# Kernel optimization log

Hardware: AMD Instinct MI355X
Metric: run time of the kernel (lower is better)

The kernel has to match this reference:

```python
import jax, jax.numpy as jnp
import numpy as np

LAG = 13
B = 32
N = 1200
NUM = 0  # self.num at call time (module starts at the init value)
H = 1.0 / 3.0


def gamma_fn(x):
    # Gamma function valid for positive and negative non-integer args
    # (reflection formula for x<0), elementwise, fp32-safe.
    xp = jnp.where(x > 0, x, jnp.float32(1.0))
    pos = jnp.exp(jax.lax.lgamma(xp))
    xn = jnp.where(x > 0, jnp.float32(0.5), x)
    neg = jnp.pi / (jnp.sin(jnp.pi * xn) * jnp.exp(jax.lax.lgamma(1.0 - xn)))
    return jnp.where(x > 0, pos, neg)


def aggregate(A, WW):
    # Fused form of: repeat_interleave -> view -> mul(WW) -> sum(dim=2) -> tanh(-x)
    # v0[l,b,i,j,e] = A[l,b,i,e]; out[l,b,j,e] = tanh(-sum_i WW[i,j,e]*A[l,b,i,e])
    return jnp.tanh(-jnp.einsum('lbie,ije->lbje', A, WW))


def setup_inputs() -> dict:
    key = jax.random.key(0)
    k = jax.random.split(key, 7)
    A = jax.random.normal(k[0], (LAG - 1, B, N, 1), jnp.float32)
    WW = jax.random.normal(k[1], (N, N, 1), jnp.float32) * 0.03
    train_init = jax.random.uniform(k[2], (B, N, LAG, 2), jnp.float32)
    alpha = jax.random.uniform(k[3], (LAG - 1, 1), jnp.float32) * 0.6 + 0.2
    fract = jax.random.uniform(k[4], (LAG - 1, 1), jnp.float32) * 0.6 + 0.2
    lambd = jax.random.normal(k[5], (LAG - 1, 1, N // 6, 1), jnp.float32) * 0.1
    l = jax.random.normal(k[6], (LAG - 1, 1, N // 6, 1), jnp.float32) * 0.1
    A_y_list = jnp.zeros((12, B, LAG - 1, N, 1), jnp.float32)
    return {"A": A, "WW": WW, "train_init": train_init, "alpha": alpha,
            "fract": fract, "lambd": lambd, "l": l, "A_y_list": A_y_list}


def reference(A, WW, train_init, alpha, fract, lambd, l, A_y_list):
    # __init__-time precomputation of A_N_OLD / A_0_NEW
    A_N_OLD = aggregate(jnp.transpose(train_init[..., :LAG - 1, 1], (2, 0, 1))[..., None], WW)
    A_0_NEW = aggregate(jnp.transpose(train_init[..., 1:LAG, 1], (2, 0, 1))[..., None], WW)

    out = aggregate(A, WW)                                   # [lag-1,B,N,1]
    A_y_list = A_y_list.at[NUM].set(jnp.transpose(out, (1, 0, 2, 3)))

    # D(): the original overwrites num=0 inside D, so only the m=0 GL term
    # survives; binom(fract,0)=Gamma(f+1)/(Gamma(1)Gamma(f+1)).
    binom0 = gamma_fn(fract + 1.0) / (gamma_fn(jnp.ones_like(fract)) * gamma_fn(fract + 1.0))
    sum_GL = A_y_list[0] * binom0[None, :, None, :]          # [B,lag-1,N,1]
    output_final_A = sum_GL / (H ** fract[None, :, None, :])

    # belta_result = sum_{k=0..3} Gamma(a+1)/(Gamma(k+1)Gamma(a-k+1))
    g_a1 = gamma_fn(alpha + 1.0)                             # [lag-1,1]
    belta_result = jnp.zeros((LAG - 1, 1), jnp.float32)
    for kk in range(4):
        kf = jnp.full((LAG - 1, 1), float(kk), jnp.float32)
        belta_result = belta_result + g_a1 / (gamma_fn(kf + 1.0) * gamma_fn(alpha - kf + 1.0))

    tmp1 = g_a1[:, None, None, :]                            # Gamma(a+1), == tmp3
    tmp2 = gamma_fn(jnp.ones((LAG - 1, 1), jnp.float32))[:, None, None, :]   # Gamma(1)=1
    tmp4 = gamma_fn(jnp.full((LAG - 1, 1), 4.0, jnp.float32))[:, None, None, :]  # Gamma(4)=6
    tmp5 = gamma_fn(alpha - 2.0)[:, None, None, :]           # Gamma(a-3+1)

    l_rep = jnp.tile(l, (1, B, 6, 1))                        # [lag-1,B,N,1]
    constant = l_rep * (tmp1 / (tmp2 * tmp1) * A_0_NEW + tmp1 / (tmp4 * tmp5) * A_N_OLD) / H
    constant = jnp.transpose(constant, (1, 0, 2, 3))         # [B,lag-1,N,1]

    lambd_rep = jnp.transpose(jnp.tile(lambd, (1, B, 6, 1)), (1, 0, 2, 3))
    return lambd_rep / belta_result[None, :, None, :] * (2.0 * output_final_A + constant)
```

## Files before the change

### kernel.cpp

```cpp
#include <hip/hip_runtime.h>
#include <math.h>

#define PI_F 3.14159265358979323846f

typedef __attribute__((ext_vector_type(8))) short bh8;
typedef __attribute__((ext_vector_type(4))) float f32x4;

#define LAG1 12
#define BB   32
#define NN   1200
#define KPAD 1216
#define NPAD 1216
#define NITER 19
#define KS0   10
#define LDSW  72


#define ROW_I4 (KPAD / 8)
#define PA_BLK 228
#define PB_BLK 150
#define PD_BLK 6
#define PC_BLK 1444
#define PE_BLK 1
#define PREP_BLOCKS (PA_BLK + PB_BLK + PD_BLK + PC_BLK + PE_BLK)

__device__ __forceinline__ unsigned short f2bf(float f) {
    unsigned int u = __float_as_uint(f);
    u = (u + 0x7fffu + ((u >> 16) & 1u)) >> 16;
    return (unsigned short)u;
}

__device__ __forceinline__ float gamma_fn_dev(float x) {
    if (x > 0.0f) return expf(lgammaf(x));
    return PI_F / (sinf(PI_F * x) * expf(lgammaf(1.0f - x)));
}

__global__ __launch_bounds__(256) void prep_kernel(const float* __restrict__ A,
                                                   const float* __restrict__ TI,
                                                   const float* __restrict__ WW,
                                                   const float* __restrict__ alpha,
                                                   const float* __restrict__ fract,
                                                   unsigned short* __restrict__ X,
                                                   unsigned short* __restrict__ WT,
                                                   float* __restrict__ coef) {
    __shared__ float tile[32][33];
    const int bid = blockIdx.x;
    const int t = threadIdx.x;

    if (bid < PA_BLK) {
        int idx = bid * 256 + t;
        int ra = idx / ROW_I4;
        int c8 = idx - ra * ROW_I4;
        int k = c8 * 8;
        int row = (ra >> 5) * 96 + ((ra >> 4) & 1) * 48 + (ra & 15);
        unsigned short v[8];
        #pragma unroll
        for (int u = 0; u < 8; u++) {
            int kk = k + u;
            v[u] = (kk < NN) ? f2bf(A[ra * NN + kk]) : (unsigned short)0;
        }
        *(int4*)&X[row * KPAD + k] = *(int4*)v;
    } else if (bid < PA_BLK + PB_BLK) {
        int idx = (bid - PA_BLK) * 256 + t;
        int b = idx / NN, i = idx - b * NN;
        const float* p = TI + (size_t)(b * NN + i) * 26 + 1;
        float vals[13];
        #pragma unroll
        for (int lg = 0; lg < 13; lg++) vals[lg] = p[lg * 2];
        int rbase = (b >> 4) * 48 + (b & 15);
        #pragma unroll
        for (int lag = 0; lag < LAG1; lag++) {
            X[(lag * 96 + rbase + 16) * KPAD + i] = f2bf(vals[lag]);
            X[(lag * 96 + rbase + 32) * KPAD + i] = f2bf(vals[lag + 1]);
        }
    } else if (bid < PA_BLK + PB_BLK + PD_BLK) {
        int idx = (bid - PA_BLK - PB_BLK) * 256 + t;
        if (idx < 768 * 2) {
            int pr = idx >> 1, h = idx & 1;
            int lag = pr / 64, rem = pr - lag * 64;
            int half = rem >> 5, gi = (rem >> 4) & 1, b16 = rem & 15;
            int row = lag * 96 + half * 48 + 16 + gi * 16 + b16;
            int4 z = {0, 0, 0, 0};
            *(int4*)&X[row * KPAD + 1200 + h * 8] = z;
        }
    } else if (bid < PA_BLK + PB_BLK + PD_BLK + PC_BLK) {
        int cb = bid - (PA_BLK + PB_BLK + PD_BLK);
        int bx = cb % 38, by = cb / 38;
        int i0 = by * 32, j0 = bx * 32;
        int tx = t & 31, ty = t >> 5;
        #pragma unroll
        for (int s = 0; s < 32; s += 8) {
            int i = i0 + ty + s, j = j0 + tx;
            tile[ty + s][tx] = (i < NN && j < NN) ? WW[i * NN + j] : 0.0f;
        }
        __syncthreads();
        #pragma unroll
        for (int s = 0; s < 32; s += 8) {
            int j = j0 + ty + s, i = i0 + tx;
            WT[j * NPAD + i] = f2bf(tile[tx][ty + s]);
        }
    } else {
        int lag = t;
        if (lag < LAG1) {
            float a = alpha[lag], f = fract[lag];
            float ga1 = expf(lgammaf(a + 1.0f));
            float belta = 0.0f;
            const float gk[4] = {1.0f, 1.0f, 2.0f, 6.0f};
            #pragma unroll
            for (int kk = 0; kk < 4; kk++)
                belta += ga1 / (gk[kk] * gamma_fn_dev(a - (float)kk + 1.0f));
            coef[lag]      = 2.0f * powf(3.0f, f);
            coef[12 + lag] = ga1 / (6.0f * gamma_fn_dev(a - 2.0f));
            coef[24 + lag] = 1.0f / belta;
        }
    }
}

__global__ __launch_bounds__(512) void gemm_splitk(const unsigned short* __restrict__ X,
                                                   const unsigned short* __restrict__ WT,
                                                   float* __restrict__ P) {
    __shared__ unsigned short Xs[2][96 * LDSW];
    __shared__ unsigned short Bs[2][64 * LDSW];
    const int bn = blockIdx.x, ks = blockIdx.y, lag = blockIdx.z;
    const int t = threadIdx.x;
    const int wave = t >> 6, lane = t & 63;
    const int l15 = lane & 15, quad = lane >> 4;
    const int mh = wave >> 2, nq = wave & 3;
    const int n0 = bn * 64;
    const int itStart = ks ? KS0 : 0;
    const int itEnd   = ks ? NITER : KS0;

    const int row0 = t >> 3, c80 = (t & 7) * 8;
    const unsigned short* gx0 = X + (size_t)(lag * 96 + row0) * KPAD + c80;
    const unsigned short* gx1 = X + (size_t)(lag * 96 + 64 + row0) * KPAD + c80;
    const unsigned short* gb0 = WT + (size_t)(n0 + row0) * NPAD + c80;
    const int lx0 = row0 * LDSW + c80;
    const int lx1 = (64 + row0) * LDSW + c80;

    int4 xr0, xr1, br0;
    {
        const int k0 = itStart * 64;
        xr0 = *(const int4*)(gx0 + k0);
        if (t < 256) xr1 = *(const int4*)(gx1 + k0);
        br0 = *(const int4*)(gb0 + k0);
    }

    f32x4 acc[3] = {};

    for (int it = itStart; it < itEnd; ++it) {
        const int p = (it - itStart) & 1;
        *(int4*)&Xs[p][lx0] = xr0;
        if (t < 256) *(int4*)&Xs[p][lx1] = xr1;
        *(int4*)&Bs[p][lx0] = br0;
        __syncthreads();
        if (it + 1 < itEnd) {
            const int k1 = (it + 1) * 64;
            xr0 = *(const int4*)(gx0 + k1);
            if (t < 256) xr1 = *(const int4*)(gx1 + k1);
            br0 = *(const int4*)(gb0 + k1);
        }
        #pragma unroll
        for (int kh = 0; kh < 2; kh++) {
            bh8 bfrag = *(const bh8*)&Bs[p][(nq * 16 + l15) * LDSW + kh * 32 + quad * 8];
            #pragma unroll
            for (int g = 0; g < 3; g++) {
                bh8 afrag = *(const bh8*)&Xs[p][(mh * 48 + g * 16 + l15) * LDSW + kh * 32 + quad * 8];
                acc[g] = __builtin_amdgcn_mfma_f32_16x16x32_bf16(afrag, bfrag, acc[g], 0, 0, 0);
            }
        }
    }

    const int j = n0 + nq * 16 + l15;
    if (j < NN) {
        float* Pk = P + (size_t)ks * (1152 * NN);
        #pragma unroll
        for (int g = 0; g < 3; g++) {
            int rowb = lag * 96 + mh * 48 + g * 16 + quad * 4;
            #pragma unroll
            for (int r = 0; r < 4; r++)
                Pk[(size_t)(rowb + r) * NN + j] = acc[g][r];
        }
    }
}

__global__ __launch_bounds__(256) void combine_kernel(const float* __restrict__ P,
                                                      const float* __restrict__ coef,
                                                      const float* __restrict__ lambd,
                                                      const float* __restrict__ l,
                                                      float* __restrict__ out) {
    int idx = blockIdx.x * 256 + threadIdx.x;
    if (idx >= BB * LAG1 * NN) return;
    int j = idx % NN;
    int t2 = idx / NN;
    int lag = t2 % LAG1, b = t2 / LAG1;
    int base = lag * 96 + (b >> 4) * 48 + (b & 15);
    const float* P1 = P + (size_t)1152 * NN;
    float s0 = P[(size_t)base * NN + j]        + P1[(size_t)base * NN + j];
    float s1 = P[(size_t)(base + 16) * NN + j] + P1[(size_t)(base + 16) * NN + j];
    float s2 = P[(size_t)(base + 32) * NN + j] + P1[(size_t)(base + 32) * NN + j];
    int jm = j % 200;
    float lv  = l[lag * 200 + jm];
    float lam = lambd[lag * 200 + jm];
    float e0 = coef[lag], c2 = coef[12 + lag], ib = coef[24 + lag];
    out[idx] = lam * ib * (e0 * tanhf(-s0) + 3.0f * lv * (tanhf(-s2) + c2 * tanhf(-s1)));
}

extern "C" void kernel_launch(void* const* d_in, const int* in_sizes, int n_in,
                              void* d_out, int out_size, void* d_ws, size_t ws_size,
                              hipStream_t stream) {
    const float* A     = (const float*)d_in[0];
    const float* WW    = (const float*)d_in[1];
    const float* TI    = (const float*)d_in[2];
    const float* alpha = (const float*)d_in[3];
    const float* fract = (const float*)d_in[4];
    const float* lambd = (const float*)d_in[5];
    const float* l     = (const float*)d_in[6];
    float* out = (float*)d_out;

    unsigned short* X  = (unsigned short*)d_ws;
    unsigned short* WT = X + 1152 * KPAD;
    float* P    = (float*)(WT + (size_t)NPAD * NPAD);
    float* coef = P + (size_t)2 * 1152 * NN;

    prep_kernel<<<PREP_BLOCKS, 256, 0, stream>>>(A, TI, WW, alpha, fract, X, WT, coef);
    gemm_splitk<<<dim3(19, 2, LAG1), 512, 0, stream>>>(X, WT, P);
    combine_kernel<<<(BB * LAG1 * NN + 255) / 256, 256, 0, stream>>>(P, coef, lambd, l, out);
}
```

Baseline: 104.1 us.

## Fuse split-K reduction and epilogue into GEMM via arrival counter; store partials in fp16

Result: slower. 254.1 us (+144.0%).

```diff
diff --git a/kernel.cpp b/kernel.cpp
--- a/kernel.cpp
+++ b/kernel.cpp
@@ -1,4 +1,5 @@
 #include <hip/hip_runtime.h>
+#include <hip/hip_fp16.h>
 #include <math.h>
 
 #define PI_F 3.14159265358979323846f
@@ -14,6 +15,7 @@
 #define NITER 19
 #define KS0   10
 #define LDSW  72
+#define NFLAG (19 * LAG1)
 
 
 #define ROW_I4 (KPAD / 8)
@@ -42,7 +44,8 @@
                                                    const float* __restrict__ fract,
                                                    unsigned short* __restrict__ X,
                                                    unsigned short* __restrict__ WT,
-                                                   float* __restrict__ coef) {
+                                                   float* __restrict__ coef,
+                                                   int* __restrict__ flags) {
     __shared__ float tile[32][33];
     const int bid = blockIdx.x;
     const int t = threadIdx.x;
@@ -100,6 +103,7 @@
             WT[j * NPAD + i] = f2bf(tile[tx][ty + s]);
         }
     } else {
+        if (t < NFLAG) flags[t] = 0;
         int lag = t;
         if (lag < LAG1) {
             float a = alpha[lag], f = fract[lag];
@@ -118,9 +122,15 @@
 
 __global__ __launch_bounds__(512) void gemm_splitk(const unsigned short* __restrict__ X,
                                                    const unsigned short* __restrict__ WT,
-                                                   float* __restrict__ P) {
+                                                   __half* __restrict__ P,
+                                                   int* __restrict__ flags,
+                                                   const float* __restrict__ coef,
+                                                   const float* __restrict__ lambd,
+                                                   const float* __restrict__ l,
+                                                   float* __restrict__ out) {
     __shared__ unsigned short Xs[2][96 * LDSW];
     __shared__ unsigned short Bs[2][64 * LDSW];
+    __shared__ int sec_flag;
     const int bn = blockIdx.x, ks = blockIdx.y, lag = blockIdx.z;
     const int t = threadIdx.x;
     const int wave = t >> 6, lane = t & 63;
@@ -171,38 +181,41 @@
     }
 
     const int j = n0 + nq * 16 + l15;
-    if (j < NN) {
-        float* Pk = P + (size_t)ks * (1152 * NN);
-        #pragma unroll
-        for (int g = 0; g < 3; g++) {
-            int rowb = lag * 96 + mh * 48 + g * 16 + quad * 4;
-            #pragma unroll
-            for (int r = 0; r < 4; r++)
-                Pk[(size_t)(rowb + r) * NN + j] = acc[g][r];
-        }
-    }
-}
-
-__global__ __launch_bounds__(256) void combine_kernel(const float* __restrict__ P,
-                                                      const float* __restrict__ coef,
-                                                      const float* __restrict__ lambd,
-                                                      const float* __restrict__ l,
-                                                      float* __restrict__ out) {
-    int idx = blockIdx.x * 256 + threadIdx.x;
-    if (idx >= BB * LAG1 * NN) return;
-    int j = idx % NN;
-    int t2 = idx / NN;
-    int lag = t2 % LAG1, b = t2 / LAG1;
-    int base = lag * 96 + (b >> 4) * 48 + (b & 15);
-    const float* P1 = P + (size_t)1152 * NN;
-    float s0 = P[(size_t)base * NN + j]        + P1[(size_t)base * NN + j];
-    float s1 = P[(size_t)(base + 16) * NN + j] + P1[(size_t)(base + 16) * NN + j];
-    float s2 = P[(size_t)(base + 32) * NN + j] + P1[(size_t)(base + 32) * NN + j];
-    int jm = j % 200;
-    float lv  = l[lag * 200 + jm];
-    float lam = lambd[lag * 200 + jm];
-    float e0 = coef[lag], c2 = coef[12 + lag], ib = coef[24 + lag];
-    out[idx] = lam * ib * (e0 * tanhf(-s0) + 3.0f * lv * (tanhf(-s2) + c2 * tanhf(-s1)));
+    {
+        __half* Pk = P + (size_t)ks * (1152 * NN);
+        if (j < NN) {
+            #pragma unroll
+            for (int g = 0; g < 3; g++) {
+                int rowb = lag * 96 + mh * 48 + g * 16 + quad * 4;
+                #pragma unroll
+                for (int r = 0; r < 4; r++)
+                    Pk[(size_t)(rowb + r) * NN + j] = __float2half(acc[g][r]);
+            }
+        }
+    }
+    __threadfence();
+    if (t == 0) sec_flag = atomicAdd(&flags[bn * LAG1 + lag], 1);
+    __syncthreads();
+    if (sec_flag == 1) {
+        __threadfence();
+        const __half* Po = P + (size_t)(1 - ks) * (1152 * NN);
+        if (j < NN) {
+            const int jm = j % 200;
+            const float lv  = l[lag * 200 + jm];
+            const float lam = lambd[lag * 200 + jm];
+            const float e0 = coef[lag], c2 = coef[12 + lag], ib = coef[24 + lag];
+            #pragma unroll
+            for (int r = 0; r < 4; r++) {
+                int rb_ = lag * 96 + mh * 48 + quad * 4 + r;
+                float s0 = acc[0][r] + __half2float(Po[(size_t)rb_ * NN + j]);
+                float s1 = acc[1][r] + __half2float(Po[(size_t)(rb_ + 16) * NN + j]);
+                float s2 = acc[2][r] + __half2float(Po[(size_t)(rb_ + 32) * NN + j]);
+                int b = mh * 16 + quad * 4 + r;
+                out[(size_t)(b * LAG1 + lag) * NN + j] =
+                    lam * ib * (e0 * tanhf(-s0) + 3.0f * lv * (tanhf(-s2) + c2 * tanhf(-s1)));
+            }
+        }
+    }
 }
 
 extern "C" void kernel_launch(void* const* d_in, const int* in_sizes, int n_in,
@@ -219,10 +232,10 @@
 
     unsigned short* X  = (unsigned short*)d_ws;
     unsigned short* WT = X + 1152 * KPAD;
-    float* P    = (float*)(WT + (size_t)NPAD * NPAD);
-    float* coef = P + (size_t)2 * 1152 * NN;
-
-    prep_kernel<<<PREP_BLOCKS, 256, 0, stream>>>(A, TI, WW, alpha, fract, X, WT, coef);
-    gemm_splitk<<<dim3(19, 2, LAG1), 512, 0, stream>>>(X, WT, P);
-    combine_kernel<<<(BB * LAG1 * NN + 255) / 256, 256, 0, stream>>>(P, coef, lambd, l, out);
-}
+    __half* P    = (__half*)(WT + (size_t)NPAD * NPAD);
+    float* coef  = (float*)(P + (size_t)2 * 1152 * NN);
+    int*   flags = (int*)(coef + 36);
+
+    prep_kernel<<<PREP_BLOCKS, 256, 0, stream>>>(A, TI, WW, alpha, fract, X, WT, coef, flags);
+    gemm_splitk<<<dim3(19, 2, LAG1), 512, 0, stream>>>(X, WT, P, flags, coef, lambd, l, out);
+}
```
